# Kernel tuning notes

Measured on AMD Instinct MI355X. Metric: run time of the kernel, lower is better.

Reference implementation:

```python
import jax, jax.numpy as jnp
import numpy as np

EPS = 1e-5  # torch LayerNorm default


def _layernorm_hd(t, gamma, beta):
    # Normalize jointly over the last two axes (n_heads, head_dim),
    # matching nn.LayerNorm((n_heads, head_dim)).
    mu = jnp.mean(t, axis=(-2, -1), keepdims=True)
    var = jnp.var(t, axis=(-2, -1), keepdims=True)
    return (t - mu) * jax.lax.rsqrt(var + EPS) * gamma + beta


def setup_inputs() -> dict:
    key = jax.random.key(0)
    B, Hs, Ws, C = 4, 256, 256, 128  # batch, spatial grid, hidden_channels
    n_heads, head_dim = 4, C // 4
    scale = (C ** 2) / n_heads  # hidden_channels**2 / n_heads, as in __init__
    ks = jax.random.split(key, 4)
    X = jax.random.normal(ks[0], (B, Hs, Ws, C), dtype=jnp.float32)
    Wq = jax.random.normal(ks[1], (C, n_heads, head_dim), dtype=jnp.float32) / scale
    Wk = jax.random.normal(ks[2], (C, n_heads, head_dim), dtype=jnp.float32) / scale
    Wv = jax.random.normal(ks[3], (C, n_heads, head_dim), dtype=jnp.float32) / scale
    # NOTE: original forward applies layernorm_key to BOTH key and value
    # (layernorm_value params are unused); we replicate that exactly.
    gamma_k = jnp.ones((n_heads, head_dim), dtype=jnp.float32)
    beta_k = jnp.zeros((n_heads, head_dim), dtype=jnp.float32)
    return {"X": X, "Wq": Wq, "Wk": Wk, "Wv": Wv, "gamma_k": gamma_k, "beta_k": beta_k}


def reference(X, Wq, Wk, Wv, gamma_k, beta_k):
    # X: [B, Hs, Ws, C]; W*: [C, h, d]
    q = jnp.einsum('bxyc,chd->bxyhd', X, Wq)
    k = jnp.einsum('bxyc,chd->bxyhd', X, Wk)
    v = jnp.einsum('bxyc,chd->bxyhd', X, Wv)
    k = _layernorm_hd(k, gamma_k, beta_k)
    v = _layernorm_hd(v, gamma_k, beta_k)  # faithful: layernorm_key used for value too
    num_points = X.shape[1] * X.shape[2]
    kv = jnp.einsum('bxyhd,bxyhe->bhde', k, v)          # tiny [B,h,d,d]
    sa = jnp.einsum('bxyhd,bhde->bxyeh', q, kv)          # note output order (e, h)
    sa = (sa / num_points).reshape(X.shape)
    return sa
```

## Files before the change

### kernel.cpp

```cpp
#include <hip/hip_runtime.h>

#define HW 65536
#define CH 128
#define NHEADS 4
#define HDIM 32
#define EPS 1e-5f
#define INV_NP (1.0f / 65536.0f)
#define INV_C (1.0f / 128.0f)

typedef float v4f __attribute__((ext_vector_type(4)));
typedef short v8s __attribute__((ext_vector_type(8)));
typedef unsigned int v4u __attribute__((ext_vector_type(4)));

__device__ __forceinline__ ushort f2bf(float f) {
    uint u = __float_as_uint(f);
    return (ushort)((u + 0x7FFFu + ((u >> 16) & 1u)) >> 16);
}

__device__ __forceinline__ v8s pack8(float4 a, float4 b) {
    v8s r;
    r[0] = (short)f2bf(a.x); r[1] = (short)f2bf(a.y);
    r[2] = (short)f2bf(a.z); r[3] = (short)f2bf(a.w);
    r[4] = (short)f2bf(b.x); r[5] = (short)f2bf(b.y);
    r[6] = (short)f2bf(b.z); r[7] = (short)f2bf(b.w);
    return r;
}

#define MFMA(a, b, c) __builtin_amdgcn_mfma_f32_16x16x32_bf16((a), (b), (c), 0, 0, 0)


__global__ __launch_bounds__(256) void prep_kernel(const float* __restrict__ Wk,
                                                   const float* __restrict__ Wv,
                                                   ushort* __restrict__ SWkT,
                                                   ushort* __restrict__ SWvT,
                                                   float* __restrict__ kv_g) {
    const int t = blockIdx.x * 256 + threadIdx.x;
    kv_g[t] = 0.f;
    kv_g[t + 8192] = 0.f;
#pragma unroll
    for (int i = 0; i < 2; ++i) {
        const int e = i * 8192 + t;
        const int c = e >> 7;
        const int row = e & 127;
        const int dst = row * 128 + (((c >> 3) + row) & 15) * 8 + (c & 7);
        SWkT[dst] = f2bf(Wk[e]);
        SWvT[dst] = f2bf(Wv[e]);
    }
}

__global__ __launch_bounds__(256, 2) void kv_kernel(const float* __restrict__ X,
                                                    const ushort* __restrict__ SWkT,
                                                    const ushort* __restrict__ SWvT,
                                                    const float* __restrict__ gamma,
                                                    const float* __restrict__ beta,
                                                    float* __restrict__ kv_g) {
    __shared__ ushort lds[40960];
    const int tid  = threadIdx.x;
    const int lane = tid & 63;
    const int w    = tid >> 6;
    const int q    = lane >> 4;
    const int ln   = lane & 15;
    const int phalf = w >> 1;
    const int isv   = w & 1;
    const int Wb    = isv ? 16384 : 0;

    const int batch  = blockIdx.x >> 7;
    const int blocal = blockIdx.x & 127;
    const float* Xb = X + ((size_t)batch * HW + (size_t)blocal * 512) * CH;

    {
        const v4u* sk = (const v4u*)SWkT;
        const v4u* sv = (const v4u*)SWvT;
        v4u* dk = (v4u*)lds;
        v4u* dv = (v4u*)(lds + 16384);
#pragma unroll
        for (int n = 0; n < 8; ++n) {
            dk[n * 256 + tid] = sk[n * 256 + tid];
            dv[n * 256 + tid] = sv[n * 256 + tid];
        }
    }

    float g8[8], be8[8];
#pragma unroll
    for (int ct = 0; ct < 8; ++ct) {
        g8[ct]  = gamma[ct * 16 + ln];
        be8[ct] = beta[ct * 16 + ln];
    }

    v4f kv00 = {0.f, 0.f, 0.f, 0.f}, kv01 = kv00, kv10 = kv00, kv11 = kv00;

    __syncthreads();

    for (int t = 0; t < 8; ++t) {
        const float* Xt = Xb + (size_t)t * 64 * CH;

        float4 xa[4][4];
#pragma unroll
        for (int ks = 0; ks < 4; ++ks) {
            const float* b0 = Xt + (phalf * 32 + ln) * CH + ks * 32 + q * 8;
            xa[ks][0] = *(const float4*)b0;
            xa[ks][1] = *(const float4*)(b0 + 4);
            xa[ks][2] = *(const float4*)(b0 + 16 * CH);
            xa[ks][3] = *(const float4*)(b0 + 16 * CH + 4);
        }
        v8s A0[4], A1[4];
#pragma unroll
        for (int ks = 0; ks < 4; ++ks) {
            A0[ks] = pack8(xa[ks][0], xa[ks][1]);
            A1[ks] = pack8(xa[ks][2], xa[ks][3]);
        }

        v4f acc[2][8];
#pragma unroll
        for (int rt = 0; rt < 2; ++rt)
#pragma unroll
            for (int ct = 0; ct < 8; ++ct) acc[rt][ct] = (v4f){0.f, 0.f, 0.f, 0.f};
#pragma unroll
        for (int ks = 0; ks < 4; ++ks) {
#pragma unroll
            for (int ct = 0; ct < 8; ++ct) {
                const int row = ct * 16 + ln;
                const v8s B = *(const v8s*)(lds + Wb + row * 128 + (((ks * 4 + q) + row) & 15) * 8);
                acc[0][ct] = MFMA(A0[ks], B, acc[0][ct]);
                acc[1][ct] = MFMA(A1[ks], B, acc[1][ct]);
            }
        }

        float mu[2][4], rs[2][4];
#pragma unroll
        for (int rt = 0; rt < 2; ++rt) {
#pragma unroll
            for (int r = 0; r < 4; ++r) {
                float s = 0.f, sq = 0.f;
#pragma unroll
                for (int ct = 0; ct < 8; ++ct) {
                    const float v = acc[rt][ct][r];
                    s += v;
                    sq += v * v;
                }
#pragma unroll
                for (int m = 1; m <= 8; m <<= 1) {
                    s  += __shfl_xor(s, m);
                    sq += __shfl_xor(sq, m);
                }
                const float m1 = s * INV_C;
                const float var = sq * INV_C - m1 * m1;
                mu[rt][r] = m1;
                rs[rt][r] = 1.0f / sqrtf(var + EPS);
            }
        }

#pragma unroll
        for (int rnd = 0; rnd < 2; ++rnd) {
            if (phalf == rnd) {
                const int base = 32768 + isv * 4096;
#pragma unroll
                for (int ct = 0; ct < 8; ++ct) {
                    const int chn = ct * 16 + ln;
#pragma unroll
                    for (int rt = 0; rt < 2; ++rt) {
#pragma unroll
                        for (int r = 0; r < 4; r += 2) {
                            const float v0 = (acc[rt][ct][r] - mu[rt][r]) * rs[rt][r] * g8[ct] + be8[ct];
                            const float v1 = (acc[rt][ct][r + 1] - mu[rt][r + 1]) * rs[rt][r + 1] * g8[ct] + be8[ct];
                            const int p32 = rt * 16 + q * 4 + r;
                            const int off = base + chn * 32 + (((p32 >> 3) + chn) & 3) * 8 + (p32 & 7);
                            *(uint*)(lds + off) = (uint)f2bf(v0) | ((uint)f2bf(v1) << 16);
                        }
                    }
                }
            }
            __syncthreads();
            {
                const int r0 = w * 32 + ln;
                const int r1 = r0 + 16;
                const v8s Ad0 = *(const v8s*)(lds + 32768 + r0 * 32 + ((q + r0) & 3) * 8);
                const v8s Ad1 = *(const v8s*)(lds + 32768 + r1 * 32 + ((q + r1) & 3) * 8);
                const v8s Be0 = *(const v8s*)(lds + 36864 + r0 * 32 + ((q + r0) & 3) * 8);
                const v8s Be1 = *(const v8s*)(lds + 36864 + r1 * 32 + ((q + r1) & 3) * 8);
                kv00 = MFMA(Ad0, Be0, kv00);
                kv01 = MFMA(Ad0, Be1, kv01);
                kv10 = MFMA(Ad1, Be0, kv10);
                kv11 = MFMA(Ad1, Be1, kv11);
            }
            __syncthreads();
        }
    }

    float* dst = kv_g + (batch * NHEADS + w) * (HDIM * HDIM);
#pragma unroll
    for (int dt = 0; dt < 2; ++dt)
#pragma unroll
        for (int et = 0; et < 2; ++et) {
            const v4f f = dt == 0 ? (et == 0 ? kv00 : kv01) : (et == 0 ? kv10 : kv11);
#pragma unroll
            for (int r = 0; r < 4; ++r) {
                const int d = dt * 16 + q * 4 + r;
                const int e = et * 16 + ln;
                atomicAdd(&dst[d * HDIM + e], f[r]);
            }
        }
}

__global__ __launch_bounds__(256) void weff_kernel(const float* __restrict__ Wq,
                                                   const float* __restrict__ kv_g,
                                                   ushort* __restrict__ SWeffT) {
    const int b = blockIdx.x >> 4;
    const int part = blockIdx.x & 15;
    const int base = part * 1024 + threadIdx.x * 4;
    const int c = base >> 7;
    const int o0 = base & 127;
    const float* kvb = kv_g + b * (NHEADS * HDIM * HDIM);
#pragma unroll
    for (int n = 0; n < 4; ++n) {
        const int o = o0 + n;
        const int h = o & 3;
        const int e = o >> 2;
        float s = 0.f;
#pragma unroll
        for (int d = 0; d < HDIM; ++d)
            s += Wq[c * CH + h * HDIM + d] * kvb[h * (HDIM * HDIM) + d * HDIM + e];
        SWeffT[b * (CH * CH) + o * 128 + (((c >> 3) + o) & 15) * 8 + (c & 7)] = f2bf(s * INV_NP);
    }
}

__global__ __launch_bounds__(256) void out_kernel(const float* __restrict__ X,
                                                  const ushort* __restrict__ SWeffT,
                                                  float* __restrict__ out) {
    __shared__ ushort lds[16384];
    const int tid  = threadIdx.x;
    const int lane = tid & 63;
    const int w    = tid >> 6;
    const int q    = lane >> 4;
    const int ln   = lane & 15;
    const int phalf = w >> 1;
    const int chalf = w & 1;

    const int batch  = blockIdx.x >> 9;
    const int blocal = blockIdx.x & 511;
    const size_t p0 = (size_t)batch * HW + (size_t)blocal * 128;

    {
        const v4u* s = (const v4u*)(SWeffT + batch * (CH * CH));
        v4u* d = (v4u*)lds;
#pragma unroll
        for (int n = 0; n < 8; ++n) d[n * 256 + tid] = s[n * 256 + tid];
    }
    __syncthreads();

    for (int t = 0; t < 2; ++t) {
        const float* Xt = X + (p0 + (size_t)t * 64) * CH;

        float4 xa[4][4];
#pragma unroll
        for (int ks = 0; ks < 4; ++ks) {
            const float* b0 = Xt + (phalf * 32 + ln) * CH + ks * 32 + q * 8;
            xa[ks][0] = *(const float4*)b0;
            xa[ks][1] = *(const float4*)(b0 + 4);
            xa[ks][2] = *(const float4*)(b0 + 16 * CH);
            xa[ks][3] = *(const float4*)(b0 + 16 * CH + 4);
        }
        v8s A0[4], A1[4];
#pragma unroll
        for (int ks = 0; ks < 4; ++ks) {
            A0[ks] = pack8(xa[ks][0], xa[ks][1]);
            A1[ks] = pack8(xa[ks][2], xa[ks][3]);
        }

        v4f acc[2][4];
#pragma unroll
        for (int rt = 0; rt < 2; ++rt)
#pragma unroll
            for (int ct = 0; ct < 4; ++ct) acc[rt][ct] = (v4f){0.f, 0.f, 0.f, 0.f};
#pragma unroll
        for (int ks = 0; ks < 4; ++ks) {
#pragma unroll
            for (int ct = 0; ct < 4; ++ct) {
                const int row = chalf * 64 + ct * 16 + ln;
                const v8s B = *(const v8s*)(lds + row * 128 + (((ks * 4 + q) + row) & 15) * 8);
                acc[0][ct] = MFMA(A0[ks], B, acc[0][ct]);
                acc[1][ct] = MFMA(A1[ks], B, acc[1][ct]);
            }
        }

        float* op = out + (p0 + (size_t)t * 64) * CH;
#pragma unroll
        for (int rt = 0; rt < 2; ++rt)
#pragma unroll
            for (int ct = 0; ct < 4; ++ct)
#pragma unroll
                for (int r = 0; r < 4; ++r) {
                    const int p = phalf * 32 + rt * 16 + q * 4 + r;
                    const int col = chalf * 64 + ct * 16 + ln;
                    op[p * CH + col] = acc[rt][ct][r];
                }
    }
}

extern "C" void kernel_launch(void* const* d_in, const int* in_sizes, int n_in,
                              void* d_out, int out_size, void* d_ws, size_t ws_size,
                              hipStream_t stream) {
    const float* X     = (const float*)d_in[0];
    const float* Wq    = (const float*)d_in[1];
    const float* Wk    = (const float*)d_in[2];
    const float* Wv    = (const float*)d_in[3];
    const float* gamma = (const float*)d_in[4];
    const float* beta  = (const float*)d_in[5];
    float* out = (float*)d_out;

    float*  kv_g   = (float*)d_ws;
    ushort* SWkT   = (ushort*)((char*)d_ws + 65536);
    ushort* SWvT   = (ushort*)((char*)d_ws + 98304);
    ushort* SWeffT = (ushort*)((char*)d_ws + 131072);

    prep_kernel<<<32, 256, 0, stream>>>(Wk, Wv, SWkT, SWvT, kv_g);
    kv_kernel<<<512, 256, 0, stream>>>(X, SWkT, SWvT, gamma, beta, kv_g);
    weff_kernel<<<64, 256, 0, stream>>>(Wq, kv_g, SWeffT);
    out_kernel<<<2048, 256, 0, stream>>>(X, SWeffT, out);
}
```

Baseline: 305.4 us.

## Restructure kv and out kernels with prefetch, packed bf16 converts and DPP reductions

Both main kernels now prefetch the next X tile into registers while computing the current one. The kv kernel has each wave compute both K and V for 16 rows instead of splitting K/V across waves, and uses hardware packed bf16 conversion, DPP row reductions instead of shuffles, and fused LayerNorm math with rsq. The out kernel swaps MFMA operand roles (weights as A, X as B) so each lane stores contiguous float4 outputs, and processes 256 points per block with fewer blocks. This raises register pressure and changes occupancy hints.

```diff
diff --git a/kernel.cpp b/kernel.cpp
--- a/kernel.cpp
+++ b/kernel.cpp
@@ -17,13 +17,32 @@
     return (ushort)((u + 0x7FFFu + ((u >> 16) & 1u)) >> 16);
 }
 
-__device__ __forceinline__ v8s pack8(float4 a, float4 b) {
-    v8s r;
-    r[0] = (short)f2bf(a.x); r[1] = (short)f2bf(a.y);
-    r[2] = (short)f2bf(a.z); r[3] = (short)f2bf(a.w);
-    r[4] = (short)f2bf(b.x); r[5] = (short)f2bf(b.y);
-    r[6] = (short)f2bf(b.z); r[7] = (short)f2bf(b.w);
+__device__ __forceinline__ uint cvtpk(float lo, float hi) {
+    uint r;
+    asm("v_cvt_pk_bf16_f32 %0, %1, %2" : "=v"(r) : "v"(lo), "v"(hi));
     return r;
+}
+
+__device__ __forceinline__ v8s pack8(const float4& a, const float4& b) {
+    union { uint u[4]; v8s s; } r;
+    r.u[0] = cvtpk(a.x, a.y);
+    r.u[1] = cvtpk(a.z, a.w);
+    r.u[2] = cvtpk(b.x, b.y);
+    r.u[3] = cvtpk(b.z, b.w);
+    return r.s;
+}
+
+template<int CTRL>
+__device__ __forceinline__ float dppadd(float x) {
+    return x + __int_as_float(
+        __builtin_amdgcn_mov_dpp(__float_as_int(x), CTRL, 0xF, 0xF, true));
+}
+__device__ __forceinline__ float red16(float x) {
+    x = dppadd<0xB1>(x);
+    x = dppadd<0x4E>(x);
+    x = dppadd<0x141>(x);
+    x = dppadd<0x140>(x);
+    return x;
 }
 
 #define MFMA(a, b, c) __builtin_amdgcn_mfma_f32_16x16x32_bf16((a), (b), (c), 0, 0, 0)
@@ -60,9 +79,6 @@
     const int w    = tid >> 6;
     const int q    = lane >> 4;
     const int ln   = lane & 15;
-    const int phalf = w >> 1;
-    const int isv   = w & 1;
-    const int Wb    = isv ? 16384 : 0;
 
     const int batch  = blockIdx.x >> 7;
     const int blocal = blockIdx.x & 127;
@@ -87,103 +103,118 @@
         be8[ct] = beta[ct * 16 + ln];
     }
 
+    int brow[8];
+#pragma unroll
+    for (int ct = 0; ct < 8; ++ct) brow[ct] = (ct * 16 + ln) * 128;
+    int bks[4];
+#pragma unroll
+    for (int ks = 0; ks < 4; ++ks) bks[ks] = ((ks * 4 + q + ln) & 15) * 8;
+    int soff[8];
+#pragma unroll
+    for (int ct = 0; ct < 8; ++ct) {
+        const int chn  = ct * 16 + ln;
+        const int slot = (((w & 1) << 1) + (q >> 1) + chn) & 3;
+        soff[ct] = chn * 32 + slot * 8 + (q & 1) * 4;
+    }
+    const int r0 = w * 32 + ln;
+    const int r1 = r0 + 16;
+    const int koff0 = r0 * 32 + ((q + r0) & 3) * 8;
+    const int koff1 = r1 * 32 + ((q + r1) & 3) * 8;
+
     v4f kv00 = {0.f, 0.f, 0.f, 0.f}, kv01 = kv00, kv10 = kv00, kv11 = kv00;
 
+    const float* xbase = Xb + (w * 16 + ln) * CH + q * 8;
+    float4 xa[8];
+#pragma unroll
+    for (int ks = 0; ks < 4; ++ks) {
+        xa[2 * ks]     = *(const float4*)(xbase + ks * 32);
+        xa[2 * ks + 1] = *(const float4*)(xbase + ks * 32 + 4);
+    }
     __syncthreads();
 
+    v8s A[4];
+#pragma unroll
+    for (int ks = 0; ks < 4; ++ks) A[ks] = pack8(xa[2 * ks], xa[2 * ks + 1]);
+
     for (int t = 0; t < 8; ++t) {
-        const float* Xt = Xb + (size_t)t * 64 * CH;
-
-        float4 xa[4][4];
+        if (t < 7) {
+            const float* xp = xbase + (size_t)(t + 1) * 64 * CH;
+#pragma unroll
+            for (int ks = 0; ks < 4; ++ks) {
+                xa[2 * ks]     = *(const float4*)(xp + ks * 32);
+                xa[2 * ks + 1] = *(const float4*)(xp + ks * 32 + 4);
+            }
+        }
+
+        v4f ak[8], av[8];
+#pragma unroll
+        for (int ct = 0; ct < 8; ++ct) {
+            ak[ct] = (v4f){0.f, 0.f, 0.f, 0.f};
+            av[ct] = (v4f){0.f, 0.f, 0.f, 0.f};
+        }
 #pragma unroll
         for (int ks = 0; ks < 4; ++ks) {
-            const float* b0 = Xt + (phalf * 32 + ln) * CH + ks * 32 + q * 8;
-            xa[ks][0] = *(const float4*)b0;
-            xa[ks][1] = *(const float4*)(b0 + 4);
-            xa[ks][2] = *(const float4*)(b0 + 16 * CH);
-            xa[ks][3] = *(const float4*)(b0 + 16 * CH + 4);
-        }
-        v8s A0[4], A1[4];
-#pragma unroll
-        for (int ks = 0; ks < 4; ++ks) {
-            A0[ks] = pack8(xa[ks][0], xa[ks][1]);
-            A1[ks] = pack8(xa[ks][2], xa[ks][3]);
-        }
-
-        v4f acc[2][8];
-#pragma unroll
-        for (int rt = 0; rt < 2; ++rt)
-#pragma unroll
-            for (int ct = 0; ct < 8; ++ct) acc[rt][ct] = (v4f){0.f, 0.f, 0.f, 0.f};
-#pragma unroll
-        for (int ks = 0; ks < 4; ++ks) {
 #pragma unroll
             for (int ct = 0; ct < 8; ++ct) {
-                const int row = ct * 16 + ln;
-                const v8s B = *(const v8s*)(lds + Wb + row * 128 + (((ks * 4 + q) + row) & 15) * 8);
-                acc[0][ct] = MFMA(A0[ks], B, acc[0][ct]);
-                acc[1][ct] = MFMA(A1[ks], B, acc[1][ct]);
-            }
-        }
-
-        float mu[2][4], rs[2][4];
-#pragma unroll
-        for (int rt = 0; rt < 2; ++rt) {
-#pragma unroll
-            for (int r = 0; r < 4; ++r) {
-                float s = 0.f, sq = 0.f;
+                const int kb = brow[ct] + bks[ks];
+                const v8s Bk = *(const v8s*)(lds + kb);
+                const v8s Bv = *(const v8s*)(lds + 16384 + kb);
+                ak[ct] = MFMA(A[ks], Bk, ak[ct]);
+                av[ct] = MFMA(A[ks], Bv, av[ct]);
+            }
+        }
+
+        float rsk[4], rsv[4], mrk[4], mrv[4];
+#pragma unroll
+        for (int r = 0; r < 4; ++r) {
+            float sk = 0.f, qk = 0.f, sv = 0.f, qv = 0.f;
+#pragma unroll
+            for (int ct = 0; ct < 8; ++ct) {
+                sk += ak[ct][r]; qk = fmaf(ak[ct][r], ak[ct][r], qk);
+                sv += av[ct][r]; qv = fmaf(av[ct][r], av[ct][r], qv);
+            }
+            sk = red16(sk); qk = red16(qk);
+            sv = red16(sv); qv = red16(qv);
+            const float mk = sk * INV_C, mv = sv * INV_C;
+            const float rk = __builtin_amdgcn_rsqf(fmaf(qk, INV_C, -mk * mk) + EPS);
+            const float rv = __builtin_amdgcn_rsqf(fmaf(qv, INV_C, -mv * mv) + EPS);
+            rsk[r] = rk; mrk[r] = mk * rk;
+            rsv[r] = rv; mrv[r] = mv * rv;
+        }
+
+#pragma unroll
+        for (int rnd = 0; rnd < 2; ++rnd) {
+            if ((w >> 1) == rnd) {
 #pragma unroll
                 for (int ct = 0; ct < 8; ++ct) {
-                    const float v = acc[rt][ct][r];
-                    s += v;
-                    sq += v * v;
-                }
-#pragma unroll
-                for (int m = 1; m <= 8; m <<= 1) {
-                    s  += __shfl_xor(s, m);
-                    sq += __shfl_xor(sq, m);
-                }
-                const float m1 = s * INV_C;
-                const float var = sq * INV_C - m1 * m1;
-                mu[rt][r] = m1;
-                rs[rt][r] = 1.0f / sqrtf(var + EPS);
-            }
-        }
-
-#pragma unroll
-        for (int rnd = 0; rnd < 2; ++rnd) {
-            if (phalf == rnd) {
-                const int base = 32768 + isv * 4096;
-#pragma unroll
-                for (int ct = 0; ct < 8; ++ct) {
-                    const int chn = ct * 16 + ln;
-#pragma unroll
-                    for (int rt = 0; rt < 2; ++rt) {
-#pragma unroll
-                        for (int r = 0; r < 4; r += 2) {
-                            const float v0 = (acc[rt][ct][r] - mu[rt][r]) * rs[rt][r] * g8[ct] + be8[ct];
-                            const float v1 = (acc[rt][ct][r + 1] - mu[rt][r + 1]) * rs[rt][r + 1] * g8[ct] + be8[ct];
-                            const int p32 = rt * 16 + q * 4 + r;
-                            const int off = base + chn * 32 + (((p32 >> 3) + chn) & 3) * 8 + (p32 & 7);
-                            *(uint*)(lds + off) = (uint)f2bf(v0) | ((uint)f2bf(v1) << 16);
-                        }
+#pragma unroll
+                    for (int r = 0; r < 4; r += 2) {
+                        const float k0 = fmaf(fmaf(ak[ct][r],     rsk[r],     -mrk[r]),     g8[ct], be8[ct]);
+                        const float k1 = fmaf(fmaf(ak[ct][r + 1], rsk[r + 1], -mrk[r + 1]), g8[ct], be8[ct]);
+                        const float v0 = fmaf(fmaf(av[ct][r],     rsv[r],     -mrv[r]),     g8[ct], be8[ct]);
+                        const float v1 = fmaf(fmaf(av[ct][r + 1], rsv[r + 1], -mrv[r + 1]), g8[ct], be8[ct]);
+                        *(uint*)(lds + 32768 + soff[ct] + r) = cvtpk(k0, k1);
+                        *(uint*)(lds + 36864 + soff[ct] + r) = cvtpk(v0, v1);
                     }
                 }
             }
             __syncthreads();
             {
-                const int r0 = w * 32 + ln;
-                const int r1 = r0 + 16;
-                const v8s Ad0 = *(const v8s*)(lds + 32768 + r0 * 32 + ((q + r0) & 3) * 8);
-                const v8s Ad1 = *(const v8s*)(lds + 32768 + r1 * 32 + ((q + r1) & 3) * 8);
-                const v8s Be0 = *(const v8s*)(lds + 36864 + r0 * 32 + ((q + r0) & 3) * 8);
-                const v8s Be1 = *(const v8s*)(lds + 36864 + r1 * 32 + ((q + r1) & 3) * 8);
+                const v8s Ad0 = *(const v8s*)(lds + 32768 + koff0);
+                const v8s Ad1 = *(const v8s*)(lds + 32768 + koff1);
+                const v8s Be0 = *(const v8s*)(lds + 36864 + koff0);
+                const v8s Be1 = *(const v8s*)(lds + 36864 + koff1);
                 kv00 = MFMA(Ad0, Be0, kv00);
                 kv01 = MFMA(Ad0, Be1, kv01);
                 kv10 = MFMA(Ad1, Be0, kv10);
                 kv11 = MFMA(Ad1, Be1, kv11);
             }
             __syncthreads();
+        }
+
+        if (t < 7) {
+#pragma unroll
+            for (int ks = 0; ks < 4; ++ks) A[ks] = pack8(xa[2 * ks], xa[2 * ks + 1]);
         }
     }
 
@@ -224,21 +255,19 @@
     }
 }
 
-__global__ __launch_bounds__(256) void out_kernel(const float* __restrict__ X,
-                                                  const ushort* __restrict__ SWeffT,
-                                                  float* __restrict__ out) {
+__global__ __launch_bounds__(256, 4) void out_kernel(const float* __restrict__ X,
+                                                     const ushort* __restrict__ SWeffT,
+                                                     float* __restrict__ out) {
     __shared__ ushort lds[16384];
     const int tid  = threadIdx.x;
     const int lane = tid & 63;
     const int w    = tid >> 6;
     const int q    = lane >> 4;
     const int ln   = lane & 15;
-    const int phalf = w >> 1;
-    const int chalf = w & 1;
-
-    const int batch  = blockIdx.x >> 9;
-    const int blocal = blockIdx.x & 511;
-    const size_t p0 = (size_t)batch * HW + (size_t)blocal * 128;
+
+    const int batch  = blockIdx.x >> 8;
+    const int blocal = blockIdx.x & 255;
+    const size_t p0 = (size_t)batch * HW + (size_t)blocal * 256;
 
     {
         const v4u* s = (const v4u*)(SWeffT + batch * (CH * CH));
@@ -246,54 +275,63 @@
 #pragma unroll
         for (int n = 0; n < 8; ++n) d[n * 256 + tid] = s[n * 256 + tid];
     }
+
+    int arow[8];
+#pragma unroll
+    for (int ot = 0; ot < 8; ++ot) arow[ot] = (ot * 16 + ln) * 128;
+    int aks[4];
+#pragma unroll
+    for (int ks = 0; ks < 4; ++ks) aks[ks] = ((ks * 4 + q + ln) & 15) * 8;
+
+    const float* xbase = X + (p0 + w * 16 + ln) * CH + q * 8;
+    float* obase       = out + (p0 + w * 16 + ln) * CH + q * 4;
+
+    float4 xa[8];
+#pragma unroll
+    for (int ks = 0; ks < 4; ++ks) {
+        xa[2 * ks]     = *(const float4*)(xbase + ks * 32);
+        xa[2 * ks + 1] = *(const float4*)(xbase + ks * 32 + 4);
+    }
     __syncthreads();
 
-    for (int t = 0; t < 2; ++t) {
-        const float* Xt = X + (p0 + (size_t)t * 64) * CH;
-
-        float4 xa[4][4];
+    v8s Bx[4];
+#pragma unroll
+    for (int ks = 0; ks < 4; ++ks) Bx[ks] = pack8(xa[2 * ks], xa[2 * ks + 1]);
+
+    for (int t = 0; t < 4; ++t) {
+        if (t < 3) {
+            const float* xp = xbase + (size_t)(t + 1) * 64 * CH;
+#pragma unroll
+            for (int ks = 0; ks < 4; ++ks) {
+                xa[2 * ks]     = *(const float4*)(xp + ks * 32);
+                xa[2 * ks + 1] = *(const float4*)(xp + ks * 32 + 4);
+            }
+        }
+
+        v4f acc[8];
+#pragma unroll
+        for (int ot = 0; ot < 8; ++ot) acc[ot] = (v4f){0.f, 0.f, 0.f, 0.f};
 #pragma unroll
         for (int ks = 0; ks < 4; ++ks) {
-            const float* b0 = Xt + (phalf * 32 + ln) * CH + ks * 32 + q * 8;
-            xa[ks][0] = *(const float4*)b0;
-            xa[ks][1] = *(const float4*)(b0 + 4);
-            xa[ks][2] = *(const float4*)(b0 + 16 * CH);
-            xa[ks][3] = *(const float4*)(b0 + 16 * CH + 4);
-        }
-        v8s A0[4], A1[4];
-#pragma unroll
-        for (int ks = 0; ks < 4; ++ks) {
-            A0[ks] = pack8(xa[ks][0], xa[ks][1]);
-            A1[ks] = pack8(xa[ks][2], xa[ks][3]);
-        }
-
-        v4f acc[2][4];
-#pragma unroll
-        for (int rt = 0; rt < 2; ++rt)
-#pragma unroll
-            for (int ct = 0; ct < 4; ++ct) acc[rt][ct] = (v4f){0.f, 0.f, 0.f, 0.f};
-#pragma unroll
-        for (int ks = 0; ks < 4; ++ks) {
-#pragma unroll
-            for (int ct = 0; ct < 4; ++ct) {
-                const int row = chalf * 64 + ct * 16 + ln;
-                const v8s B = *(const v8s*)(lds + row * 128 + (((ks * 4 + q) + row) & 15) * 8);
-                acc[0][ct] = MFMA(A0[ks], B, acc[0][ct]);
-                acc[1][ct] = MFMA(A1[ks], B, acc[1][ct]);
-            }
-        }
-
-        float* op = out + (p0 + (size_t)t * 64) * CH;
-#pragma unroll
-        for (int rt = 0; rt < 2; ++rt)
-#pragma unroll
-            for (int ct = 0; ct < 4; ++ct)
-#pragma unroll
-                for (int r = 0; r < 4; ++r) {
-                    const int p = phalf * 32 + rt * 16 + q * 4 + r;
-                    const int col = chalf * 64 + ct * 16 + ln;
-                    op[p * CH + col] = acc[rt][ct][r];
-                }
+#pragma unroll
+            for (int ot = 0; ot < 8; ++ot) {
+                const v8s Aw = *(const v8s*)(lds + arow[ot] + aks[ks]);
+                acc[ot] = MFMA(Aw, Bx[ks], acc[ot]);
+            }
+        }
+
+        float* op = obase + (size_t)t * 64 * CH;
+#pragma unroll
+        for (int ot = 0; ot < 8; ++ot) {
+            float4 s;
+            s.x = acc[ot][0]; s.y = acc[ot][1]; s.z = acc[ot][2]; s.w = acc[ot][3];
+            *(float4*)(op + ot * 16) = s;
+        }
+
+        if (t < 3) {
+#pragma unroll
+            for (int ks = 0; ks < 4; ++ks) Bx[ks] = pack8(xa[2 * ks], xa[2 * ks + 1]);
+        }
     }
 }
 
@@ -316,5 +354,5 @@
     prep_kernel<<<32, 256, 0, stream>>>(Wk, Wv, SWkT, SWvT, kv_g);
     kv_kernel<<<512, 256, 0, stream>>>(X, SWkT, SWvT, gamma, beta, kv_g);
     weff_kernel<<<64, 256, 0, stream>>>(Wq, kv_g, SWeffT);
-    out_kernel<<<2048, 256, 0, stream>>>(X, SWeffT, out);
-}
+    out_kernel<<<1024, 256, 0, stream>>>(X, SWeffT, out);
+}
```

Measured after the change: 279.1 us. 1.09x faster.
